# Performance work log

Measured on AMD Instinct MI355X. Metric: run time of the kernel, lower is better.

The kernel has to match this reference:

```python
import jax, jax.numpy as jnp
import numpy as np

N = 50000    # nodes per batched graph
E = 800000   # edges per batched graph
G = 256      # graphs in batch
DIN, DH, NGF = 64, 128, 4


def _gcn_encode(x, src, dst, gid, Ws, bs):
    # DGL GraphConv, norm='both': out = D_in^{-1/2} A (D_out^{-1/2} X W) + b, then ReLU
    ones_e = jnp.ones(src.shape[0], x.dtype)
    deg_out = jnp.clip(jax.ops.segment_sum(ones_e, src, num_segments=N), 1.0)
    deg_in = jnp.clip(jax.ops.segment_sum(ones_e, dst, num_segments=N), 1.0)
    nsrc = deg_out ** -0.5  # [N]
    ndst = deg_in ** -0.5   # [N]
    h = x
    for W, b in zip(Ws, bs):
        h = (h * nsrc[:, None]) @ W                       # [N, DH]
        m = jax.ops.segment_sum(h[src], dst, num_segments=N)  # gather-scatter over edges
        h = jax.nn.relu(m * ndst[:, None] + b)
    # AvgPooling: per-graph mean of node features
    cnt = jnp.clip(jax.ops.segment_sum(jnp.ones(N, x.dtype), gid, num_segments=G), 1.0)
    return jax.ops.segment_sum(h, gid, num_segments=G) / cnt[:, None]  # [G, DH]


def setup_inputs() -> dict:
    key = jax.random.key(0)
    ks = jax.random.split(key, 24)
    s = 1.0 / np.sqrt(DIN)
    sh = 1.0 / np.sqrt(DH)
    inp = {
        'solute_x': jax.random.normal(ks[0], (N, DIN), jnp.float32),
        'solvent_x': jax.random.normal(ks[1], (N, DIN), jnp.float32),
        'global_feats': jax.random.normal(ks[2], (G, NGF), jnp.float32),
        'solute_src': jax.random.randint(ks[3], (E,), 0, N, jnp.int32),
        'solute_dst': jax.random.randint(ks[4], (E,), 0, N, jnp.int32),
        'solvent_src': jax.random.randint(ks[5], (E,), 0, N, jnp.int32),
        'solvent_dst': jax.random.randint(ks[6], (E,), 0, N, jnp.int32),
        'solute_gid': jnp.sort(jax.random.randint(ks[7], (N,), 0, G, jnp.int32)),
        'solvent_gid': jnp.sort(jax.random.randint(ks[8], (N,), 0, G, jnp.int32)),
    }
    # solute encoder params
    inp['su_W0'] = jax.random.uniform(ks[9], (DIN, DH), jnp.float32, -s, s)
    inp['su_W1'] = jax.random.uniform(ks[10], (DH, DH), jnp.float32, -sh, sh)
    inp['su_W2'] = jax.random.uniform(ks[11], (DH, DH), jnp.float32, -sh, sh)
    inp['su_b'] = jnp.zeros((3, DH), jnp.float32)
    # solvent encoder params
    inp['sv_W0'] = jax.random.uniform(ks[12], (DIN, DH), jnp.float32, -s, s)
    inp['sv_W1'] = jax.random.uniform(ks[13], (DH, DH), jnp.float32, -sh, sh)
    inp['sv_W2'] = jax.random.uniform(ks[14], (DH, DH), jnp.float32, -sh, sh)
    inp['sv_b'] = jnp.zeros((3, DH), jnp.float32)
    # MLP head: (2*DH + NGF) -> 128 -> 64 -> 1
    d0 = 2 * DH + NGF
    inp['mlp_W0'] = jax.random.uniform(ks[15], (d0, 128), jnp.float32, -1/np.sqrt(d0), 1/np.sqrt(d0))
    inp['mlp_b0'] = jnp.zeros((128,), jnp.float32)
    inp['mlp_W1'] = jax.random.uniform(ks[16], (128, 64), jnp.float32, -1/np.sqrt(128), 1/np.sqrt(128))
    inp['mlp_b1'] = jnp.zeros((64,), jnp.float32)
    inp['mlp_W2'] = jax.random.uniform(ks[17], (64, 1), jnp.float32, -1/8.0, 1/8.0)
    inp['mlp_b2'] = jnp.zeros((1,), jnp.float32)
    return inp


def reference(solute_x, solvent_x, global_feats, solute_src, solute_dst,
              solvent_src, solvent_dst, solute_gid, solvent_gid,
              su_W0, su_W1, su_W2, su_b, sv_W0, sv_W1, sv_W2, sv_b,
              mlp_W0, mlp_b0, mlp_W1, mlp_b1, mlp_W2, mlp_b2):
    su = _gcn_encode(solute_x, solute_src, solute_dst, solute_gid,
                     [su_W0, su_W1, su_W2], [su_b[0], su_b[1], su_b[2]])
    sv = _gcn_encode(solvent_x, solvent_src, solvent_dst, solvent_gid,
                     [sv_W0, sv_W1, sv_W2], [sv_b[0], sv_b[1], sv_b[2]])
    comb = jnp.concatenate([su, sv, global_feats], axis=1)  # [G, 2*DH+NGF]
    h = jax.nn.relu(comb @ mlp_W0 + mlp_b0)  # dropout = identity (eval)
    h = jax.nn.relu(h @ mlp_W1 + mlp_b1)
    return h @ mlp_W2 + mlp_b2  # [G, 1]
```

## Files before the change

### kernel.cpp

```cpp
#include <hip/hip_runtime.h>


#define DHID 128
#define CHUNK 1600
#define SB 32

static __device__ __forceinline__ void fma4(float4& o, float a, const float4& w) {
  o.x = fmaf(a, w.x, o.x);
  o.y = fmaf(a, w.y, o.y);
  o.z = fmaf(a, w.z, o.z);
  o.w = fmaf(a, w.w, o.w);
}
static __device__ __forceinline__ void add4(float4& o, const float4& v) {
  o.x += v.x; o.y += v.y; o.z += v.z; o.w += v.w;
}

__global__ __launch_bounds__(256) void hist_kernel(
    const int* __restrict__ src, const int* __restrict__ dst,
    unsigned short* __restrict__ parts, int E, int es) {
  __shared__ unsigned int h[CHUNK];
  const int t = threadIdx.x;
  const int slice = blockIdx.x;
  const int chunk = blockIdx.y;
  const int arr = blockIdx.z;
  for (int i = t; i < CHUNK; i += 256) h[i] = 0;
  __syncthreads();
  const int* __restrict__ idx = arr ? dst : src;
  const int base = chunk * CHUNK;
  const int e0 = slice * es;
  const int e1 = min(e0 + es, E);
  int e = e0 + t;
  for (; e + 768 < e1; e += 1024) {
    int i0 = idx[e], i1 = idx[e + 256], i2 = idx[e + 512], i3 = idx[e + 768];
    unsigned v0 = (unsigned)(i0 - base);
    unsigned v1 = (unsigned)(i1 - base);
    unsigned v2 = (unsigned)(i2 - base);
    unsigned v3 = (unsigned)(i3 - base);
    if (v0 < CHUNK) atomicAdd(&h[v0], 1u);
    if (v1 < CHUNK) atomicAdd(&h[v1], 1u);
    if (v2 < CHUNK) atomicAdd(&h[v2], 1u);
    if (v3 < CHUNK) atomicAdd(&h[v3], 1u);
  }
  for (; e < e1; e += 256) {
    unsigned v = (unsigned)(idx[e] - base);
    if (v < CHUNK) atomicAdd(&h[v], 1u);
  }
  __syncthreads();
  unsigned short* p = parts + (((size_t)arr * gridDim.y + chunk) * SB + slice) * CHUNK;
  for (int i = t; i < CHUNK; i += 256) p[i] = (unsigned short)h[i];
}

__global__ __launch_bounds__(256) void reduce_kernel(
    unsigned short* __restrict__ parts,
    int* __restrict__ deg_in, float* __restrict__ nsrc, float* __restrict__ ndst,
    int* __restrict__ sp, int N, int nch) {
  const int t = threadIdx.x;
  const int n = blockIdx.x * 256 + t;
  int sumD = 0;
  if (n < N) {
    const int chunk = n / CHUNK;
    const int local = n % CHUNK;
    const size_t strideA = (size_t)nch * SB * CHUNK;
    const unsigned short* __restrict__ pS = parts + ((size_t)chunk * SB) * CHUNK + local;
    unsigned short* __restrict__ pD = parts + strideA + ((size_t)chunk * SB) * CHUNK + local;
    int sumS = 0;
    #pragma unroll
    for (int s = 0; s < SB; ++s) sumS += (int)pS[(size_t)s * CHUNK];
    unsigned short vD[SB];
    #pragma unroll
    for (int s = 0; s < SB; ++s) vD[s] = pD[(size_t)s * CHUNK];
    #pragma unroll
    for (int s = 0; s < SB; ++s) {
      int c = (int)vD[s];
      vD[s] = (unsigned short)sumD;
      sumD += c;
    }
    #pragma unroll
    for (int s = 0; s < SB; ++s) pD[(size_t)s * CHUNK] = vD[s];
    deg_in[n] = sumD;
    nsrc[n] = 1.0f / sqrtf((float)max(sumS, 1));
    ndst[n] = 1.0f / sqrtf((float)max(sumD, 1));
  }
  int v = sumD;
  #pragma unroll
  for (int d = 32; d > 0; d >>= 1) v += __shfl_xor(v, d);
  __shared__ int ws[4];
  if ((t & 63) == 0) ws[t >> 6] = v;
  __syncthreads();
  if (t == 0) sp[blockIdx.x] = ws[0] + ws[1] + ws[2] + ws[3];
}

__global__ void scan_mid(int* __restrict__ part, int* __restrict__ total_out, int nb) {
  const int tid = threadIdx.x;
  const int lane = tid & 63;
  const int wv = tid >> 6;
  int v = (tid < nb) ? part[tid] : 0;
  int x = v;
  #pragma unroll
  for (int d = 1; d < 64; d <<= 1) {
    int y = __shfl_up(x, d);
    if (lane >= d) x += y;
  }
  __shared__ int ws[4];
  if (lane == 63) ws[wv] = x;
  __syncthreads();
  int woff = 0;
  for (int k = 0; k < wv; ++k) woff += ws[k];
  if (tid < nb) part[tid] = woff + x - v;
  if (tid == 255) *total_out = woff + x;
}

__global__ void scan_final(const int* __restrict__ deg, const int* __restrict__ part,
                           int* __restrict__ rowptr, int n) {
  const int tid = threadIdx.x;
  const int i = blockIdx.x * 256 + tid;
  const int lane = tid & 63;
  const int wv = tid >> 6;
  int v = (i < n) ? deg[i] : 0;
  int x = v;
  #pragma unroll
  for (int d = 1; d < 64; d <<= 1) {
    int y = __shfl_up(x, d);
    if (lane >= d) x += y;
  }
  __shared__ int ws[4];
  if (lane == 63) ws[wv] = x;
  __syncthreads();
  int woff = 0;
  for (int k = 0; k < wv; ++k) woff += ws[k];
  if (i < n) rowptr[i] = part[blockIdx.x] + woff + x - v;
}

__global__ __launch_bounds__(256) void fillrank_kernel(
    const int* __restrict__ src, const int* __restrict__ dst,
    const unsigned short* __restrict__ partD, const int* __restrict__ rowptr,
    int* __restrict__ colidx, int E, int es) {
  __shared__ unsigned int h[CHUNK];
  const int t = threadIdx.x;
  const int slice = blockIdx.x;
  const int chunk = blockIdx.y;
  for (int i = t; i < CHUNK; i += 256) h[i] = 0;
  __syncthreads();
  const int base = chunk * CHUNK;
  const unsigned short* __restrict__ po = partD + ((size_t)chunk * SB + slice) * CHUNK;
  const int e0 = slice * es;
  const int e1 = min(e0 + es, E);
  for (int e = e0 + t; e < e1; e += 256) {
    int d = dst[e];
    unsigned v = (unsigned)(d - base);
    if (v < CHUNK) {
      int rank = (int)atomicAdd(&h[v], 1u);
      int slot = rowptr[d] + (int)po[v] + rank;
      colidx[slot] = src[e];
    }
  }
}

#define BM 128
#define BKC 32
__global__ __launch_bounds__(256) void gemm_scaled(
    const float* __restrict__ A, const float* __restrict__ W,
    const float* __restrict__ nsrc, float* __restrict__ out,
    int nrows, int K) {
  __shared__ __align__(16) float As[BM][BKC + 4];
  __shared__ __align__(16) float Ws[BKC][DHID];
  const int tid = threadIdx.x;
  const int row0 = blockIdx.x * BM;
  const int cx = tid & 15;
  const int ry = tid >> 4;
  const int lr = tid >> 1;
  const int lk = (tid & 1) * 16;
  const int wk = tid >> 3;
  const int wc = (tid & 7) * 4;

  float4 acc[8][2];
  #pragma unroll
  for (int r = 0; r < 8; ++r) {
    acc[r][0] = make_float4(0.f, 0.f, 0.f, 0.f);
    acc[r][1] = make_float4(0.f, 0.f, 0.f, 0.f);
  }

  const int arow = row0 + lr;
  const float scale = (arow < nrows) ? nsrc[arow] : 0.f;

  for (int k0 = 0; k0 < K; k0 += BKC) {
    if (arow < nrows) {
      const float4* ap = (const float4*)(A + (size_t)arow * K + k0 + lk);
      #pragma unroll
      for (int j = 0; j < 4; ++j) {
        float4 v = ap[j];
        v.x *= scale; v.y *= scale; v.z *= scale; v.w *= scale;
        *(float4*)&As[lr][lk + j * 4] = v;
      }
    } else {
      #pragma unroll
      for (int j = 0; j < 4; ++j)
        *(float4*)&As[lr][lk + j * 4] = make_float4(0.f, 0.f, 0.f, 0.f);
    }
    {
      const float* wp = W + (size_t)(k0 + wk) * DHID;
      #pragma unroll
      for (int j = 0; j < 4; ++j)
        *(float4*)&Ws[wk][wc + j * 32] = *(const float4*)(wp + wc + j * 32);
    }
    __syncthreads();
    #pragma unroll 4
    for (int kk = 0; kk < BKC; kk += 2) {
      float4 w00 = *(float4*)&Ws[kk][cx * 4];
      float4 w01 = *(float4*)&Ws[kk][64 + cx * 4];
      float4 w10 = *(float4*)&Ws[kk + 1][cx * 4];
      float4 w11 = *(float4*)&Ws[kk + 1][64 + cx * 4];
      #pragma unroll
      for (int r = 0; r < 8; ++r) {
        float2 a = *(float2*)&As[ry + 16 * r][kk];
        fma4(acc[r][0], a.x, w00);
        fma4(acc[r][1], a.x, w01);
        fma4(acc[r][0], a.y, w10);
        fma4(acc[r][1], a.y, w11);
      }
    }
    __syncthreads();
  }
  #pragma unroll
  for (int r = 0; r < 8; ++r) {
    int row = row0 + ry + 16 * r;
    if (row < nrows) {
      float* op = out + (size_t)row * DHID;
      *(float4*)(op + cx * 4) = acc[r][0];
      *(float4*)(op + 64 + cx * 4) = acc[r][1];
    }
  }
}

__global__ void agg_kernel(const float* __restrict__ hB, const int* __restrict__ rowptr,
                           const int* __restrict__ colidx, const float* __restrict__ ndst,
                           const float* __restrict__ bias, float* __restrict__ out, int N) {
  int wid = (blockIdx.x * blockDim.x + threadIdx.x) >> 6;
  int lane = threadIdx.x & 63;
  if (wid >= N) return;
  int beg = rowptr[wid];
  int end = rowptr[wid + 1];
  const int half = lane >> 5;
  const int col = (lane & 31) * 4;
  float4 acc = make_float4(0.f, 0.f, 0.f, 0.f);

  for (int c0 = beg; c0 < end; c0 += 64) {
    int cnt = min(end - c0, 64);
    int myidx = (lane < cnt) ? colidx[c0 + lane] : 0;
    int pairs = cnt >> 1;
    int j = 0;
    for (; j + 4 <= pairs; j += 4) {
      int s0 = __shfl(myidx, 2 * j + half);
      int s1 = __shfl(myidx, 2 * j + 2 + half);
      int s2 = __shfl(myidx, 2 * j + 4 + half);
      int s3 = __shfl(myidx, 2 * j + 6 + half);
      float4 v0 = *(const float4*)(hB + (size_t)s0 * DHID + col);
      float4 v1 = *(const float4*)(hB + (size_t)s1 * DHID + col);
      float4 v2 = *(const float4*)(hB + (size_t)s2 * DHID + col);
      float4 v3 = *(const float4*)(hB + (size_t)s3 * DHID + col);
      add4(acc, v0); add4(acc, v1); add4(acc, v2); add4(acc, v3);
    }
    for (; j < pairs; ++j) {
      int s = __shfl(myidx, 2 * j + half);
      float4 v = *(const float4*)(hB + (size_t)s * DHID + col);
      add4(acc, v);
    }
    if (cnt & 1) {
      int s = __shfl(myidx, cnt - 1);
      if (half == 0) {
        float4 v = *(const float4*)(hB + (size_t)s * DHID + col);
        add4(acc, v);
      }
    }
  }
  acc.x += __shfl_xor(acc.x, 32);
  acc.y += __shfl_xor(acc.y, 32);
  acc.z += __shfl_xor(acc.z, 32);
  acc.w += __shfl_xor(acc.w, 32);
  if (half == 0) {
    float nd = ndst[wid];
    float4 b = *(const float4*)(bias + col);
    float4 o;
    o.x = fmaxf(fmaf(acc.x, nd, b.x), 0.f);
    o.y = fmaxf(fmaf(acc.y, nd, b.y), 0.f);
    o.z = fmaxf(fmaf(acc.z, nd, b.z), 0.f);
    o.w = fmaxf(fmaf(acc.w, nd, b.w), 0.f);
    *(float4*)(out + (size_t)wid * DHID + col) = o;
  }
}

__global__ void pool_kernel(const float* __restrict__ h, const int* __restrict__ gid,
                            float* __restrict__ pooled, int* __restrict__ cnt,
                            int N, int C) {
  int wid = (blockIdx.x * blockDim.x + threadIdx.x) >> 6;
  int lane = threadIdx.x & 63;
  int n0 = wid * C;
  if (n0 >= N) return;
  int n1 = min(n0 + C, N);
  int gcur = gid[n0];
  int runcnt = 0;
  float2 acc = make_float2(0.f, 0.f);
  for (int nd = n0; nd < n1; ++nd) {
    int g = gid[nd];
    if (g != gcur) {
      atomicAdd(&pooled[(size_t)gcur * DHID + lane * 2], acc.x);
      atomicAdd(&pooled[(size_t)gcur * DHID + lane * 2 + 1], acc.y);
      if (lane == 0) atomicAdd(&cnt[gcur], runcnt);
      acc = make_float2(0.f, 0.f);
      runcnt = 0;
      gcur = g;
    }
    const float2 v = *(const float2*)(h + (size_t)nd * DHID + lane * 2);
    acc.x += v.x;
    acc.y += v.y;
    ++runcnt;
  }
  atomicAdd(&pooled[(size_t)gcur * DHID + lane * 2], acc.x);
  atomicAdd(&pooled[(size_t)gcur * DHID + lane * 2 + 1], acc.y);
  if (lane == 0) atomicAdd(&cnt[gcur], runcnt);
}

__global__ void mlp_kernel(const float* __restrict__ psu, const float* __restrict__ psv,
                           const int* __restrict__ cnt_su, const int* __restrict__ cnt_sv,
                           const float* __restrict__ gf,
                           const float* __restrict__ W0, const float* __restrict__ b0,
                           const float* __restrict__ W1, const float* __restrict__ b1,
                           const float* __restrict__ W2, const float* __restrict__ b2,
                           float* __restrict__ out) {
  int g = blockIdx.x;
  int t = threadIdx.x;
  __shared__ float comb[260];
  __shared__ float h0[128];
  __shared__ float h1[64];
  float inv_su = 1.0f / (float)max(cnt_su[g], 1);
  float inv_sv = 1.0f / (float)max(cnt_sv[g], 1);
  comb[t] = psu[(size_t)g * DHID + t] * inv_su;
  comb[128 + t] = psv[(size_t)g * DHID + t] * inv_sv;
  if (t < 4) comb[256 + t] = gf[g * 4 + t];
  __syncthreads();
  float acc = b0[t];
  for (int k = 0; k < 260; ++k) acc = fmaf(comb[k], W0[k * 128 + t], acc);
  h0[t] = fmaxf(acc, 0.f);
  __syncthreads();
  if (t < 64) {
    float a = b1[t];
    for (int k = 0; k < 128; ++k) a = fmaf(h0[k], W1[k * 64 + t], a);
    h1[t] = fmaxf(a, 0.f);
  }
  __syncthreads();
  if (t < 64) {
    float p = h1[t] * W2[t];
    #pragma unroll
    for (int d = 32; d > 0; d >>= 1) p += __shfl_down(p, d);
    if (t == 0) out[g] = p + b2[0];
  }
}

extern "C" void kernel_launch(void* const* d_in, const int* in_sizes, int n_in,
                              void* d_out, int out_size, void* d_ws, size_t ws_size,
                              hipStream_t stream) {
  const float* solute_x  = (const float*)d_in[0];
  const float* solvent_x = (const float*)d_in[1];
  const float* gfeat     = (const float*)d_in[2];
  const int* su_src = (const int*)d_in[3];
  const int* su_dst = (const int*)d_in[4];
  const int* sv_src = (const int*)d_in[5];
  const int* sv_dst = (const int*)d_in[6];
  const int* su_gid = (const int*)d_in[7];
  const int* sv_gid = (const int*)d_in[8];
  const float* enc_W[2][3] = {
    {(const float*)d_in[9],  (const float*)d_in[10], (const float*)d_in[11]},
    {(const float*)d_in[13], (const float*)d_in[14], (const float*)d_in[15]}};
  const float* enc_b[2] = {(const float*)d_in[12], (const float*)d_in[16]};
  const float* mW0 = (const float*)d_in[17];
  const float* mb0 = (const float*)d_in[18];
  const float* mW1 = (const float*)d_in[19];
  const float* mb1 = (const float*)d_in[20];
  const float* mW2 = (const float*)d_in[21];
  const float* mb2 = (const float*)d_in[22];

  const int N = in_sizes[0] / 64;
  const int E = in_sizes[3];
  const int G = in_sizes[2] / 4;

  const int* srcs[2] = {su_src, sv_src};
  const int* dsts[2] = {su_dst, sv_dst};
  const int* gids[2] = {su_gid, sv_gid};
  const float* xs[2] = {solute_x, solvent_x};

  char* ws = (char*)d_ws;
  size_t off = 0;
  auto alloc = [&](size_t bytes) -> void* {
    void* p = ws + off;
    off = (off + bytes + 255) & ~(size_t)255;
    return p;
  };
  const int NB = (N + 255) / 256;
  const int NCH = (N + CHUNK - 1) / CHUNK;
  const int RB = (NCH * CHUNK + 255) / 256;
  const int ES = (E + SB - 1) / SB;
  const size_t arrStride = (size_t)NCH * SB * CHUNK;

  int*   deg_in  = (int*)alloc((size_t)N * 4);
  float* nsrc    = (float*)alloc((size_t)N * 4);
  float* ndst    = (float*)alloc((size_t)N * 4);
  int*   rowptr  = (int*)alloc((size_t)(N + 1) * 4);
  int*   sp      = (int*)alloc((size_t)RB * 4);
  unsigned short* parts = (unsigned short*)alloc(2 * arrStride * 2);
  int*   colidx  = (int*)alloc((size_t)E * 4);
  float* bufA    = (float*)alloc((size_t)N * DHID * 4);
  float* bufB    = (float*)alloc((size_t)N * DHID * 4);
  float* pbase   = (float*)alloc(((size_t)2 * G * DHID + 2 * G) * 4);
  float* pooled_su = pbase;
  float* pooled_sv = pbase + (size_t)G * DHID;
  int*   cnt_su    = (int*)(pbase + (size_t)2 * G * DHID);
  int*   cnt_sv    = cnt_su + G;
  (void)ws_size; (void)n_in; (void)out_size;

  float* pooleds[2] = {pooled_su, pooled_sv};
  int*   cnts[2]    = {cnt_su, cnt_sv};

  hipMemsetAsync(pbase, 0, ((size_t)2 * G * DHID + 2 * G) * 4, stream);

  const int TB = 256;
  const int ggrid = (N + BM - 1) / BM;
  const int agrid = (N + 3) / 4;
  const int PC = 25;
  const int pwaves = (N + PC - 1) / PC;
  const int pgrid = (pwaves + 3) / 4;

  for (int enc = 0; enc < 2; ++enc) {
    hist_kernel<<<dim3(SB, NCH, 2), TB, 0, stream>>>(srcs[enc], dsts[enc], parts, E, ES);
    reduce_kernel<<<RB, TB, 0, stream>>>(parts, deg_in, nsrc, ndst, sp, N, NCH);
    scan_mid<<<1, 256, 0, stream>>>(sp, rowptr + N, NB);
    scan_final<<<NB, 256, 0, stream>>>(deg_in, sp, rowptr, N);
    fillrank_kernel<<<dim3(SB, NCH), TB, 0, stream>>>(srcs[enc], dsts[enc],
                                                      parts + arrStride, rowptr,
                                                      colidx, E, ES);

    const float* in = xs[enc];
    int K = 64;
    for (int l = 0; l < 3; ++l) {
      gemm_scaled<<<ggrid, TB, 0, stream>>>(in, enc_W[enc][l], nsrc, bufB, N, K);
      agg_kernel<<<agrid, TB, 0, stream>>>(bufB, rowptr, colidx, ndst,
                                           enc_b[enc] + l * DHID, bufA, N);
      in = bufA;
      K = DHID;
    }
    pool_kernel<<<pgrid, TB, 0, stream>>>(bufA, gids[enc], pooleds[enc], cnts[enc], N, PC);
  }

  mlp_kernel<<<G, 128, 0, stream>>>(pooled_su, pooled_sv, cnt_su, cnt_sv, gfeat,
                                    mW0, mb0, mW1, mb1, mW2, mb2, (float*)d_out);
}
```

Measured before the change: 666.2 us.

## Batch solute and solvent encoders into shared launches via grid dimension

Both GCN encoders now run in the same kernel launches, with the encoder index taken from an extra grid dimension and per-encoder workspace strides. This halves the number of launches and doubles the blocks per launch, so small kernels like scans and reduce fill the GPU better and launch gaps shrink. The workspace is carved for two encoders, with the parts histogram buffer aliased onto bufB. If the workspace is too small, the code falls back to the sequential per-encoder path.

```diff
diff --git a/kernel.cpp b/kernel.cpp
--- a/kernel.cpp
+++ b/kernel.cpp
@@ -16,16 +16,19 @@
 }
 
 __global__ __launch_bounds__(256) void hist_kernel(
-    const int* __restrict__ src, const int* __restrict__ dst,
-    unsigned short* __restrict__ parts, int E, int es) {
+    const int* __restrict__ src0, const int* __restrict__ dst0,
+    const int* __restrict__ src1, const int* __restrict__ dst1,
+    unsigned short* __restrict__ parts, int E, int es, size_t encPS) {
   __shared__ unsigned int h[CHUNK];
   const int t = threadIdx.x;
   const int slice = blockIdx.x;
   const int chunk = blockIdx.y;
-  const int arr = blockIdx.z;
+  const int arr = blockIdx.z & 1;
+  const int enc = blockIdx.z >> 1;
   for (int i = t; i < CHUNK; i += 256) h[i] = 0;
   __syncthreads();
-  const int* __restrict__ idx = arr ? dst : src;
+  const int* __restrict__ idx = arr ? (enc ? dst1 : dst0) : (enc ? src1 : src0);
+  unsigned short* __restrict__ pe = parts + (size_t)enc * encPS;
   const int base = chunk * CHUNK;
   const int e0 = slice * es;
   const int e1 = min(e0 + es, E);
@@ -46,14 +49,21 @@
     if (v < CHUNK) atomicAdd(&h[v], 1u);
   }
   __syncthreads();
-  unsigned short* p = parts + (((size_t)arr * gridDim.y + chunk) * SB + slice) * CHUNK;
+  unsigned short* p = pe + (((size_t)arr * gridDim.y + chunk) * SB + slice) * CHUNK;
   for (int i = t; i < CHUNK; i += 256) p[i] = (unsigned short)h[i];
 }
 
 __global__ __launch_bounds__(256) void reduce_kernel(
     unsigned short* __restrict__ parts,
     int* __restrict__ deg_in, float* __restrict__ nsrc, float* __restrict__ ndst,
-    int* __restrict__ sp, int N, int nch) {
+    int* __restrict__ sp, int N, int nch,
+    size_t encPS, size_t sN, size_t sSP) {
+  const int enc = blockIdx.y;
+  parts += (size_t)enc * encPS;
+  deg_in += (size_t)enc * sN;
+  nsrc += (size_t)enc * sN;
+  ndst += (size_t)enc * sN;
+  sp += (size_t)enc * sSP;
   const int t = threadIdx.x;
   const int n = blockIdx.x * 256 + t;
   int sumD = 0;
@@ -90,7 +100,11 @@
   if (t == 0) sp[blockIdx.x] = ws[0] + ws[1] + ws[2] + ws[3];
 }
 
-__global__ void scan_mid(int* __restrict__ part, int* __restrict__ total_out, int nb) {
+__global__ void scan_mid(int* __restrict__ sp, int* __restrict__ rowptr,
+                         int nb, int N, size_t sSP, size_t sRP) {
+  const int enc = blockIdx.x;
+  int* part = sp + (size_t)enc * sSP;
+  int* total_out = rowptr + (size_t)enc * sRP + N;
   const int tid = threadIdx.x;
   const int lane = tid & 63;
   const int wv = tid >> 6;
@@ -110,8 +124,13 @@
   if (tid == 255) *total_out = woff + x;
 }
 
-__global__ void scan_final(const int* __restrict__ deg, const int* __restrict__ part,
-                           int* __restrict__ rowptr, int n) {
+__global__ void scan_final(const int* __restrict__ deg, const int* __restrict__ sp,
+                           int* __restrict__ rowptr, int n,
+                           size_t sN, size_t sSP, size_t sRP) {
+  const int enc = blockIdx.y;
+  deg += (size_t)enc * sN;
+  const int* part = sp + (size_t)enc * sSP;
+  rowptr += (size_t)enc * sRP;
   const int tid = threadIdx.x;
   const int i = blockIdx.x * 256 + tid;
   const int lane = tid & 63;
@@ -128,19 +147,27 @@
   __syncthreads();
   int woff = 0;
   for (int k = 0; k < wv; ++k) woff += ws[k];
-  if (i < n) rowptr[i] = part[blockIdx.x] + woff + x - v;
+  if (i < n) rowptr[i] = part[blockIdx.y == enc ? blockIdx.x : blockIdx.x] + woff + x - v;
 }
 
 __global__ __launch_bounds__(256) void fillrank_kernel(
-    const int* __restrict__ src, const int* __restrict__ dst,
-    const unsigned short* __restrict__ partD, const int* __restrict__ rowptr,
-    int* __restrict__ colidx, int E, int es) {
+    const int* __restrict__ src0, const int* __restrict__ dst0,
+    const int* __restrict__ src1, const int* __restrict__ dst1,
+    const unsigned short* __restrict__ parts, const int* __restrict__ rowptr,
+    int* __restrict__ colidx, int E, int es,
+    size_t encPS, size_t arrStride, size_t sRP, size_t sE) {
   __shared__ unsigned int h[CHUNK];
   const int t = threadIdx.x;
   const int slice = blockIdx.x;
   const int chunk = blockIdx.y;
+  const int enc = blockIdx.z;
   for (int i = t; i < CHUNK; i += 256) h[i] = 0;
   __syncthreads();
+  const int* __restrict__ src = enc ? src1 : src0;
+  const int* __restrict__ dst = enc ? dst1 : dst0;
+  const unsigned short* __restrict__ partD = parts + (size_t)enc * encPS + arrStride;
+  rowptr += (size_t)enc * sRP;
+  colidx += (size_t)enc * sE;
   const int base = chunk * CHUNK;
   const unsigned short* __restrict__ po = partD + ((size_t)chunk * SB + slice) * CHUNK;
   const int e0 = slice * es;
@@ -159,9 +186,15 @@
 #define BM 128
 #define BKC 32
 __global__ __launch_bounds__(256) void gemm_scaled(
-    const float* __restrict__ A, const float* __restrict__ W,
+    const float* __restrict__ A0, const float* __restrict__ A1,
+    const float* __restrict__ W0p, const float* __restrict__ W1p,
     const float* __restrict__ nsrc, float* __restrict__ out,
-    int nrows, int K) {
+    int nrows, int K, size_t sN, size_t sNH) {
+  const int enc = blockIdx.y;
+  const float* __restrict__ A = enc ? A1 : A0;
+  const float* __restrict__ W = enc ? W1p : W0p;
+  nsrc += (size_t)enc * sN;
+  out += (size_t)enc * sNH;
   __shared__ __align__(16) float As[BM][BKC + 4];
   __shared__ __align__(16) float Ws[BKC][DHID];
   const int tid = threadIdx.x;
@@ -234,7 +267,16 @@
 
 __global__ void agg_kernel(const float* __restrict__ hB, const int* __restrict__ rowptr,
                            const int* __restrict__ colidx, const float* __restrict__ ndst,
-                           const float* __restrict__ bias, float* __restrict__ out, int N) {
+                           const float* __restrict__ bias0, const float* __restrict__ bias1,
+                           float* __restrict__ out, int N,
+                           size_t sNH, size_t sRP, size_t sE, size_t sN) {
+  const int enc = blockIdx.y;
+  hB += (size_t)enc * sNH;
+  rowptr += (size_t)enc * sRP;
+  colidx += (size_t)enc * sE;
+  ndst += (size_t)enc * sN;
+  out += (size_t)enc * sNH;
+  const float* __restrict__ bias = enc ? bias1 : bias0;
   int wid = (blockIdx.x * blockDim.x + threadIdx.x) >> 6;
   int lane = threadIdx.x & 63;
   if (wid >= N) return;
@@ -289,9 +331,16 @@
   }
 }
 
-__global__ void pool_kernel(const float* __restrict__ h, const int* __restrict__ gid,
+__global__ void pool_kernel(const float* __restrict__ h,
+                            const int* __restrict__ gid0, const int* __restrict__ gid1,
                             float* __restrict__ pooled, int* __restrict__ cnt,
-                            int N, int C) {
+                            int N, int C, int G,
+                            size_t sNH) {
+  const int enc = blockIdx.y;
+  h += (size_t)enc * sNH;
+  const int* __restrict__ gid = enc ? gid1 : gid0;
+  pooled += (size_t)enc * G * DHID;
+  cnt += (size_t)enc * G;
   int wid = (blockIdx.x * blockDim.x + threadIdx.x) >> 6;
   int lane = threadIdx.x & 63;
   int n0 = wid * C;
@@ -388,37 +437,49 @@
   const int* gids[2] = {su_gid, sv_gid};
   const float* xs[2] = {solute_x, solvent_x};
 
-  char* ws = (char*)d_ws;
-  size_t off = 0;
-  auto alloc = [&](size_t bytes) -> void* {
-    void* p = ws + off;
-    off = (off + bytes + 255) & ~(size_t)255;
-    return p;
-  };
   const int NB = (N + 255) / 256;
   const int NCH = (N + CHUNK - 1) / CHUNK;
   const int RB = (NCH * CHUNK + 255) / 256;
   const int ES = (E + SB - 1) / SB;
   const size_t arrStride = (size_t)NCH * SB * CHUNK;
-
-  int*   deg_in  = (int*)alloc((size_t)N * 4);
-  float* nsrc    = (float*)alloc((size_t)N * 4);
-  float* ndst    = (float*)alloc((size_t)N * 4);
-  int*   rowptr  = (int*)alloc((size_t)(N + 1) * 4);
-  int*   sp      = (int*)alloc((size_t)RB * 4);
-  unsigned short* parts = (unsigned short*)alloc(2 * arrStride * 2);
-  int*   colidx  = (int*)alloc((size_t)E * 4);
-  float* bufA    = (float*)alloc((size_t)N * DHID * 4);
-  float* bufB    = (float*)alloc((size_t)N * DHID * 4);
-  float* pbase   = (float*)alloc(((size_t)2 * G * DHID + 2 * G) * 4);
+  const size_t encPS = 2 * arrStride;
+
+  char* ws = (char*)d_ws;
+  int*   deg_in; float* nsrc; float* ndst; int* rowptr; int* sp;
+  int*   colidx; float* bufA; unsigned short* parts; float* bufB;
+  float* pbase;
+  size_t total = 0;
+  int NE = 2;
+  auto carve = [&](int ne) -> size_t {
+    size_t off = 0;
+    auto alloc = [&](size_t bytes) -> void* {
+      void* p = ws + off;
+      off = (off + bytes + 255) & ~(size_t)255;
+      return p;
+    };
+    deg_in = (int*)alloc((size_t)ne * N * 4);
+    nsrc   = (float*)alloc((size_t)ne * N * 4);
+    ndst   = (float*)alloc((size_t)ne * N * 4);
+    rowptr = (int*)alloc((size_t)ne * (N + 1) * 4);
+    sp     = (int*)alloc((size_t)ne * RB * 4);
+    colidx = (int*)alloc((size_t)ne * E * 4);
+    bufA   = (float*)alloc((size_t)ne * N * DHID * 4);
+    size_t partsB = (size_t)ne * encPS * 2;
+    size_t bufBB  = (size_t)ne * N * DHID * 4;
+    char* uni = (char*)alloc(partsB > bufBB ? partsB : bufBB);
+    parts = (unsigned short*)uni;
+    bufB  = (float*)uni;
+    pbase = (float*)alloc(((size_t)2 * G * DHID + 2 * G) * 4);
+    return off;
+  };
+  total = carve(2);
+  if (total > ws_size) { NE = 1; total = carve(1); }
+  (void)n_in; (void)out_size;
+
   float* pooled_su = pbase;
   float* pooled_sv = pbase + (size_t)G * DHID;
   int*   cnt_su    = (int*)(pbase + (size_t)2 * G * DHID);
   int*   cnt_sv    = cnt_su + G;
-  (void)ws_size; (void)n_in; (void)out_size;
-
-  float* pooleds[2] = {pooled_su, pooled_sv};
-  int*   cnts[2]    = {cnt_su, cnt_sv};
 
   hipMemsetAsync(pbase, 0, ((size_t)2 * G * DHID + 2 * G) * 4, stream);
 
@@ -429,25 +490,61 @@
   const int pwaves = (N + PC - 1) / PC;
   const int pgrid = (pwaves + 3) / 4;
 
-  for (int enc = 0; enc < 2; ++enc) {
-    hist_kernel<<<dim3(SB, NCH, 2), TB, 0, stream>>>(srcs[enc], dsts[enc], parts, E, ES);
-    reduce_kernel<<<RB, TB, 0, stream>>>(parts, deg_in, nsrc, ndst, sp, N, NCH);
-    scan_mid<<<1, 256, 0, stream>>>(sp, rowptr + N, NB);
-    scan_final<<<NB, 256, 0, stream>>>(deg_in, sp, rowptr, N);
-    fillrank_kernel<<<dim3(SB, NCH), TB, 0, stream>>>(srcs[enc], dsts[enc],
-                                                      parts + arrStride, rowptr,
-                                                      colidx, E, ES);
-
-    const float* in = xs[enc];
+  if (NE == 2) {
+    const size_t sN = N, sRP = N + 1, sSP = RB, sE = E, sNH = (size_t)N * DHID;
+    hist_kernel<<<dim3(SB, NCH, 4), TB, 0, stream>>>(
+        su_src, su_dst, sv_src, sv_dst, parts, E, ES, encPS);
+    reduce_kernel<<<dim3(RB, 2), TB, 0, stream>>>(
+        parts, deg_in, nsrc, ndst, sp, N, NCH, encPS, sN, sSP);
+    scan_mid<<<2, 256, 0, stream>>>(sp, rowptr, NB, N, sSP, sRP);
+    scan_final<<<dim3(NB, 2), 256, 0, stream>>>(deg_in, sp, rowptr, N, sN, sSP, sRP);
+    fillrank_kernel<<<dim3(SB, NCH, 2), TB, 0, stream>>>(
+        su_src, su_dst, sv_src, sv_dst, parts, rowptr, colidx, E, ES,
+        encPS, arrStride, sRP, sE);
+
+    const float* A0 = xs[0];
+    const float* A1 = xs[1];
     int K = 64;
     for (int l = 0; l < 3; ++l) {
-      gemm_scaled<<<ggrid, TB, 0, stream>>>(in, enc_W[enc][l], nsrc, bufB, N, K);
-      agg_kernel<<<agrid, TB, 0, stream>>>(bufB, rowptr, colidx, ndst,
-                                           enc_b[enc] + l * DHID, bufA, N);
-      in = bufA;
+      gemm_scaled<<<dim3(ggrid, 2), TB, 0, stream>>>(
+          A0, A1, enc_W[0][l], enc_W[1][l], nsrc, bufB, N, K, sN, sNH);
+      agg_kernel<<<dim3(agrid, 2), TB, 0, stream>>>(
+          bufB, rowptr, colidx, ndst, enc_b[0] + l * DHID, enc_b[1] + l * DHID,
+          bufA, N, sNH, sRP, sE, sN);
+      A0 = bufA;
+      A1 = bufA + sNH;
       K = DHID;
     }
-    pool_kernel<<<pgrid, TB, 0, stream>>>(bufA, gids[enc], pooleds[enc], cnts[enc], N, PC);
+    pool_kernel<<<dim3(pgrid, 2), TB, 0, stream>>>(
+        bufA, su_gid, sv_gid, pooled_su, cnt_su, N, PC, G, sNH);
+  } else {
+    float* pooleds[2] = {pooled_su, pooled_sv};
+    int*   cnts[2]    = {cnt_su, cnt_sv};
+    for (int enc = 0; enc < 2; ++enc) {
+      hist_kernel<<<dim3(SB, NCH, 2), TB, 0, stream>>>(
+          srcs[enc], dsts[enc], srcs[enc], dsts[enc], parts, E, ES, 0);
+      reduce_kernel<<<dim3(RB, 1), TB, 0, stream>>>(
+          parts, deg_in, nsrc, ndst, sp, N, NCH, 0, 0, 0);
+      scan_mid<<<1, 256, 0, stream>>>(sp, rowptr, NB, N, 0, 0);
+      scan_final<<<dim3(NB, 1), 256, 0, stream>>>(deg_in, sp, rowptr, N, 0, 0, 0);
+      fillrank_kernel<<<dim3(SB, NCH, 1), TB, 0, stream>>>(
+          srcs[enc], dsts[enc], srcs[enc], dsts[enc], parts, rowptr, colidx,
+          E, ES, 0, arrStride, 0, 0);
+
+      const float* in = xs[enc];
+      int K = 64;
+      for (int l = 0; l < 3; ++l) {
+        gemm_scaled<<<dim3(ggrid, 1), TB, 0, stream>>>(
+            in, in, enc_W[enc][l], enc_W[enc][l], nsrc, bufB, N, K, 0, 0);
+        agg_kernel<<<dim3(agrid, 1), TB, 0, stream>>>(
+            bufB, rowptr, colidx, ndst, enc_b[enc] + l * DHID, enc_b[enc] + l * DHID,
+            bufA, N, 0, 0, 0, 0);
+        in = bufA;
+        K = DHID;
+      }
+      pool_kernel<<<dim3(pgrid, 1), TB, 0, stream>>>(
+          bufA, gids[enc], gids[enc], pooleds[enc], cnts[enc], N, PC, G, 0);
+    }
   }
 
   mlp_kernel<<<G, 128, 0, stream>>>(pooled_su, pooled_sv, cnt_su, cnt_sv, gfeat,
```

Measured after the change: 582.7 us. -12.5%, faster.
